# Kernel optimization log

Measured on AMD Instinct MI355X. Metric: run time of the kernel, lower is better.

## Reference

```python
import jax, jax.numpy as jnp
import numpy as np

TOP_K = 2
HEAD_NUM = 16


def setup_inputs() -> dict:
    key = jax.random.key(0)
    ks = jax.random.split(key, 6)
    B, H, N, D, G = 8, HEAD_NUM, 2048, 64, 128
    return {
        "q": jax.random.normal(ks[0], (B, H, N, D), dtype=jnp.float32),
        "k": jax.random.normal(ks[1], (B, H, N, D), dtype=jnp.float32),
        "v": jax.random.normal(ks[2], (B, H, N, D), dtype=jnp.float32),
        "gating_input": jax.random.normal(ks[3], (B, N, G), dtype=jnp.float32),
        "rank3_ninf_mask": jnp.zeros((B, N, N), dtype=jnp.float32),
        "W_gate": jax.random.normal(ks[4], (H, G), dtype=jnp.float32) * 0.02,
        "b_gate": jnp.zeros((H,), dtype=jnp.float32),
    }


def reference(q, k, v, gating_input, rank3_ninf_mask, W_gate, b_gate):
    B = q.shape[0]
    d = q.shape[-1]
    # --- router ---
    gate_logits = gating_input.mean(axis=1) @ W_gate.T + b_gate      # [B, H]
    gate_softmax = jax.nn.softmax(gate_logits, axis=1)               # [B, H]
    _, top_k_idx = jax.lax.top_k(gate_softmax, TOP_K)                # [B, K]
    gating_mask = jnp.zeros_like(gate_softmax).at[
        jnp.arange(B)[:, None], top_k_idx].set(1.0)
    # load balancing loss
    tokens_per_expert = gating_mask.sum(axis=0)                      # [H]
    density = tokens_per_expert / (tokens_per_expert.sum() + 1e-6)
    lb_loss = HEAD_NUM * jnp.sum(gate_softmax.mean(axis=0) * density)
    # --- gather selected heads: [B, K, N, D] ---
    idx = top_k_idx[:, :, None, None]
    q_sel = jnp.take_along_axis(q, idx, axis=1)
    k_sel = jnp.take_along_axis(k, idx, axis=1)
    v_sel = jnp.take_along_axis(v, idx, axis=1)
    # --- scaled dot attention ---
    score = jnp.einsum('bhqd,bhkd->bhqk', q_sel, k_sel) / jnp.sqrt(
        jnp.asarray(d, dtype=q.dtype))                               # [B,K,N,N]
    score = score + rank3_ninf_mask[:, None, :, :]
    weights = jax.nn.softmax(score, axis=3)
    out = jnp.einsum('bhqk,bhkd->bhqd', weights, v_sel)              # [B,K,N,D]
    B_, K_, N_, D_ = out.shape
    out = out.transpose(0, 2, 1, 3).reshape(B_, N_, K_ * D_)         # [B,N,K*D]
    return out, lb_loss
```

## Files before the change

### kernel.cpp

```cpp
#include <hip/hip_runtime.h>

#define NSEQ 2048
#define DH 64
#define NH 16
#define BKV 64
#define PSTRIDE 8448

typedef __attribute__((ext_vector_type(8))) short bf16x8;
typedef __attribute__((ext_vector_type(4))) short s16x4;
typedef __attribute__((ext_vector_type(4))) float f32x4;
typedef __attribute__((ext_vector_type(16))) float f32x16;
typedef __attribute__((ext_vector_type(4))) unsigned u32x4;

static __device__ __forceinline__ short f2bf(float f) {
    __bf16 b = (__bf16)f;
    return __builtin_bit_cast(short, b);
}

__global__ void gate_partial(const float* __restrict__ gi, float* __restrict__ wsA, int SL) {
    int b = blockIdx.x / SL, sl = blockIdx.x % SL;
    int rows = NSEQ / SL;
    int tid = threadIdx.x;
    int g = tid & 127, half = tid >> 7;
    float s = 0.f;
    int n0 = sl * rows;
    for (int n = n0 + half; n < n0 + rows; n += 2)
        s += gi[((size_t)b * NSEQ + n) * 128 + g];
    __shared__ float part[2][128];
    part[half][g] = s;
    __syncthreads();
    if (tid < 128) wsA[(b * SL + sl) * 128 + tid] = part[0][tid] + part[1][tid];
}

__global__ void gate_final(const float* __restrict__ wsA, const float* __restrict__ Wg,
                           const float* __restrict__ bg, float* __restrict__ ws_sm,
                           int* __restrict__ ws_idx, int SL) {
    int b = blockIdx.x, tid = threadIdx.x;
    __shared__ float meanv[128];
    __shared__ float logits[NH];
    if (tid < 128) {
        float s = 0.f;
        for (int sl = 0; sl < SL; ++sl) s += wsA[(b * SL + sl) * 128 + tid];
        meanv[tid] = s * (1.0f / NSEQ);
    }
    __syncthreads();
    if (tid < 128) {
        int h = tid >> 3, j = tid & 7;
        float p = 0.f;
        for (int i = 0; i < 16; ++i) { int g = j + 8 * i; p += meanv[g] * Wg[h * 128 + g]; }
        p += __shfl_xor(p, 1);
        p += __shfl_xor(p, 2);
        p += __shfl_xor(p, 4);
        if (j == 0) logits[h] = p + bg[h];
    }
    __syncthreads();
    if (tid == 0) {
        float mx = logits[0];
        for (int h = 1; h < NH; ++h) mx = fmaxf(mx, logits[h]);
        float e[NH], sum = 0.f;
        for (int h = 0; h < NH; ++h) { e[h] = __expf(logits[h] - mx); sum += e[h]; }
        float inv = 1.0f / sum;
        for (int h = 0; h < NH; ++h) ws_sm[b * NH + h] = e[h] * inv;
        int i1 = 0;
        for (int h = 1; h < NH; ++h) if (logits[h] > logits[i1]) i1 = h;
        int i2 = (i1 == 0) ? 1 : 0;
        for (int h = 0; h < NH; ++h) if (h != i1 && logits[h] > logits[i2]) i2 = h;
        ws_idx[b * 2 + 0] = i1;
        ws_idx[b * 2 + 1] = i2;
    }
}

static __device__ __forceinline__ void lb_compute(const float* ws_sm, const int* ws_idx,
                                                  float* out_lb) {
    float counts[NH];
    for (int h = 0; h < NH; ++h) counts[h] = 0.f;
    for (int i = 0; i < 16; ++i) counts[ws_idx[i]] += 1.0f;
    float lb = 0.f;
    for (int h = 0; h < NH; ++h) {
        float msm = 0.f;
        for (int b = 0; b < 8; ++b) msm += ws_sm[b * NH + h];
        msm *= (1.0f / 8.0f);
        lb += msm * (counts[h] / (16.0f + 1e-6f));
    }
    out_lb[0] = lb * (float)NH;
}

__global__ void lb_kernel(const float* __restrict__ ws_sm, const int* __restrict__ ws_idx,
                          float* __restrict__ out_lb) {
    if (threadIdx.x == 0 && blockIdx.x == 0) lb_compute(ws_sm, ws_idx, out_lb);
}

template<int SPLIT>
__global__ __launch_bounds__(256, 3)
void attn_kernel(const float* __restrict__ q, const float* __restrict__ k,
                 const float* __restrict__ v, const float* __restrict__ mask,
                 const int* __restrict__ topk, float* __restrict__ out,
                 float* __restrict__ part) {
    const int qt = blockIdx.x & 15;
    const int sp = blockIdx.x >> 4;
    const int kk = blockIdx.y;
    const int b  = blockIdx.z;
    const int hh = topk[b * 2 + kk];
    const int tid = threadIdx.x;
    const int wave = tid >> 6;
    const int lane = tid & 63;
    const int lq = lane & 31;
    const int hi = lane >> 5;

    const int nt = 32 / SPLIT;
    const int t_begin = sp * nt;

    __shared__ short Kb[64][72];
    __shared__ short Vt[64][72];
    __shared__ float scb[4][32];

    const float QSC = 0.125f * 1.4426950408889634f;
    const float MSC = 1.4426950408889634f;
    const float THR = 10.0f;

    const size_t headoff = ((size_t)b * NH + hh) * (size_t)NSEQ * DH;
    const int qbase = qt * 128 + wave * 32;

    bf16x8 qf[4];
    {
        const float* qp = q + headoff + (size_t)(qbase + lq) * DH;
        #pragma unroll
        for (int dk = 0; dk < 4; ++dk) {
            const float* p = qp + dk * 16 + hi * 8;
            float4 a = *(const float4*)p;
            float4 c = *(const float4*)(p + 4);
            bf16x8 f = { f2bf(a.x * QSC), f2bf(a.y * QSC), f2bf(a.z * QSC), f2bf(a.w * QSC),
                         f2bf(c.x * QSC), f2bf(c.y * QSC), f2bf(c.z * QSC), f2bf(c.w * QSC) };
            qf[dk] = f;
        }
    }

    f32x16 acc0, acc1;
    #pragma unroll
    for (int r = 0; r < 16; ++r) { acc0[r] = 0.f; acc1[r] = 0.f; }
    float m_r = -1e30f, l_r = 0.f;

    const float* kb = k + headoff;
    const float* vb = v + headoff;
    const float* mb = mask + (size_t)b * NSEQ * NSEQ + (size_t)(qbase + lq) * NSEQ;

    const int krow = tid >> 3;
    const int kcol = (tid & 7) * 8;
    const int vrow = (tid & 15) * 4;
    const int vcol = (tid >> 4) * 4;

    float4 kreg[4], vreg[4], mreg[8];

    auto issue_kv = [&](int t0) {
        const float* kp = kb + (size_t)(t0 + krow) * DH + kcol;
        kreg[0] = *(const float4*)kp;
        kreg[1] = *(const float4*)(kp + 4);
        kreg[2] = *(const float4*)(kp + 32 * DH);
        kreg[3] = *(const float4*)(kp + 32 * DH + 4);
        const float* vp = vb + (size_t)(t0 + vrow) * DH + vcol;
        #pragma unroll
        for (int i = 0; i < 4; ++i) vreg[i] = *(const float4*)(vp + i * DH);
    };
    auto issue_mask = [&](int t0) {
        const float* mp = mb + t0 + hi * 4;
        #pragma unroll
        for (int g = 0; g < 4; ++g) {
            mreg[g]     = *(const float4*)(mp + g * 8);
            mreg[4 + g] = *(const float4*)(mp + 32 + g * 8);
        }
    };

    auto pack2 = [&](float a, float bb) -> unsigned {
        union { short s[2]; unsigned u; } t;
        t.s[0] = f2bf(a); t.s[1] = f2bf(bb);
        return t.u;
    };
    auto buildfrag = [&](float a0, float a1, float a2, float a3,
                         float a4, float a5, float a6, float a7) -> bf16x8 {
        unsigned pk01 = pack2(a0, a1), pk23 = pack2(a2, a3);
        unsigned pk45 = pack2(a4, a5), pk67 = pack2(a6, a7);
        unsigned ta = hi ? pk01 : pk45;
        unsigned tb = hi ? pk23 : pk67;
        unsigned ya = __shfl_xor(ta, 32);
        unsigned yb = __shfl_xor(tb, 32);
        u32x4 fr = { hi ? ya : pk01, hi ? yb : pk23,
                     hi ? pk45 : ya, hi ? pk67 : yb };
        return __builtin_bit_cast(bf16x8, fr);
    };

    issue_kv(t_begin * BKV);
    issue_mask(t_begin * BKV);

    for (int t = 0; t < nt; ++t) {
        const int t0 = (t_begin + t) * BKV;
        __syncthreads();
        {
            bf16x8 k0 = { f2bf(kreg[0].x), f2bf(kreg[0].y), f2bf(kreg[0].z), f2bf(kreg[0].w),
                          f2bf(kreg[1].x), f2bf(kreg[1].y), f2bf(kreg[1].z), f2bf(kreg[1].w) };
            bf16x8 k1 = { f2bf(kreg[2].x), f2bf(kreg[2].y), f2bf(kreg[2].z), f2bf(kreg[2].w),
                          f2bf(kreg[3].x), f2bf(kreg[3].y), f2bf(kreg[3].z), f2bf(kreg[3].w) };
            *(bf16x8*)&Kb[krow][kcol] = k0;
            *(bf16x8*)&Kb[krow + 32][kcol] = k1;
            s16x4 c0v = { f2bf(vreg[0].x), f2bf(vreg[1].x), f2bf(vreg[2].x), f2bf(vreg[3].x) };
            s16x4 c1v = { f2bf(vreg[0].y), f2bf(vreg[1].y), f2bf(vreg[2].y), f2bf(vreg[3].y) };
            s16x4 c2v = { f2bf(vreg[0].z), f2bf(vreg[1].z), f2bf(vreg[2].z), f2bf(vreg[3].z) };
            s16x4 c3v = { f2bf(vreg[0].w), f2bf(vreg[1].w), f2bf(vreg[2].w), f2bf(vreg[3].w) };
            *(s16x4*)&Vt[vcol + 0][vrow] = c0v;
            *(s16x4*)&Vt[vcol + 1][vrow] = c1v;
            *(s16x4*)&Vt[vcol + 2][vrow] = c2v;
            *(s16x4*)&Vt[vcol + 3][vrow] = c3v;
        }
        __syncthreads();

        f32x16 S0, S1;
        #pragma unroll
        for (int r = 0; r < 16; ++r) { S0[r] = 0.f; S1[r] = 0.f; }
        #pragma unroll
        for (int dk = 0; dk < 4; ++dk) {
            bf16x8 kf0 = *(const bf16x8*)&Kb[lq][dk * 16 + hi * 8];
            bf16x8 kf1 = *(const bf16x8*)&Kb[32 + lq][dk * 16 + hi * 8];
            S0 = __builtin_amdgcn_mfma_f32_32x32x16_bf16(kf0, qf[dk], S0, 0, 0, 0);
            S1 = __builtin_amdgcn_mfma_f32_32x32x16_bf16(kf1, qf[dk], S1, 0, 0, 0);
        }
        #pragma unroll
        for (int g = 0; g < 4; ++g) {
            S0[4*g+0] = fmaf(mreg[g].x, MSC, S0[4*g+0]);
            S0[4*g+1] = fmaf(mreg[g].y, MSC, S0[4*g+1]);
            S0[4*g+2] = fmaf(mreg[g].z, MSC, S0[4*g+2]);
            S0[4*g+3] = fmaf(mreg[g].w, MSC, S0[4*g+3]);
            S1[4*g+0] = fmaf(mreg[4+g].x, MSC, S1[4*g+0]);
            S1[4*g+1] = fmaf(mreg[4+g].y, MSC, S1[4*g+1]);
            S1[4*g+2] = fmaf(mreg[4+g].z, MSC, S1[4*g+2]);
            S1[4*g+3] = fmaf(mreg[4+g].w, MSC, S1[4*g+3]);
        }

        if (t + 1 < nt) issue_kv(t0 + BKV);

        float tmx[16];
        #pragma unroll
        for (int r = 0; r < 16; ++r) tmx[r] = fmaxf(S0[r], S1[r]);
        #pragma unroll
        for (int w2 = 8; w2 > 0; w2 >>= 1)
            #pragma unroll
            for (int r = 0; r < 8; ++r) if (r < w2) tmx[r] = fmaxf(tmx[r], tmx[r + w2]);
        float pm = fmaxf(tmx[0], __shfl_xor(tmx[0], 32));

        if (__any(pm > m_r + THR)) {
            float mnew = fmaxf(m_r, pm);
            float scw = __builtin_amdgcn_exp2f(m_r - mnew);
            if (lane < 32) scb[wave][lane] = scw;
            #pragma unroll
            for (int g = 0; g < 4; ++g) {
                float4 s4 = *(const float4*)&scb[wave][hi * 4 + g * 8];
                acc0[4*g+0] *= s4.x; acc1[4*g+0] *= s4.x;
                acc0[4*g+1] *= s4.y; acc1[4*g+1] *= s4.y;
                acc0[4*g+2] *= s4.z; acc1[4*g+2] *= s4.z;
                acc0[4*g+3] *= s4.w; acc1[4*g+3] *= s4.w;
            }
            l_r *= scw; m_r = mnew;
        }
        float ps = 0.f;
        #pragma unroll
        for (int r = 0; r < 16; ++r) { float p = __builtin_amdgcn_exp2f(S0[r] - m_r); ps += p; S0[r] = p; }
        #pragma unroll
        for (int r = 0; r < 16; ++r) { float p = __builtin_amdgcn_exp2f(S1[r] - m_r); ps += p; S1[r] = p; }
        ps += __shfl_xor(ps, 32);
        l_r += ps;

        bf16x8 pf0 = buildfrag(S0[0], S0[1], S0[2],  S0[3],  S0[4],  S0[5],  S0[6],  S0[7]);
        bf16x8 pf1 = buildfrag(S0[8], S0[9], S0[10], S0[11], S0[12], S0[13], S0[14], S0[15]);
        bf16x8 pf2 = buildfrag(S1[0], S1[1], S1[2],  S1[3],  S1[4],  S1[5],  S1[6],  S1[7]);
        bf16x8 pf3 = buildfrag(S1[8], S1[9], S1[10], S1[11], S1[12], S1[13], S1[14], S1[15]);

        if (t + 1 < nt) issue_mask(t0 + BKV);

        #pragma unroll
        for (int c = 0; c < 4; ++c) {
            bf16x8 pf = (c == 0) ? pf0 : (c == 1) ? pf1 : (c == 2) ? pf2 : pf3;
            bf16x8 vf0 = *(const bf16x8*)&Vt[lq][c * 16 + hi * 8];
            bf16x8 vf1 = *(const bf16x8*)&Vt[32 + lq][c * 16 + hi * 8];
            acc0 = __builtin_amdgcn_mfma_f32_32x32x16_bf16(pf, vf0, acc0, 0, 0, 0);
            acc1 = __builtin_amdgcn_mfma_f32_32x32x16_bf16(pf, vf1, acc1, 0, 0, 0);
        }
    }

    if (SPLIT == 1) {
        if (lane < 32) scb[wave][lane] = 1.0f / l_r;
        #pragma unroll
        for (int g = 0; g < 4; ++g) {
            float4 s4 = *(const float4*)&scb[wave][hi * 4 + g * 8];
            #pragma unroll
            for (int j = 0; j < 4; ++j) {
                int qrow = qbase + hi * 4 + g * 8 + j;
                float sc = (j == 0) ? s4.x : (j == 1) ? s4.y : (j == 2) ? s4.z : s4.w;
                float* op = out + ((size_t)b * NSEQ + qrow) * 128 + kk * 64;
                op[lq]      = acc0[4*g+j] * sc;
                op[32 + lq] = acc1[4*g+j] * sc;
            }
        }
    } else {
        float* pp = part + (size_t)((((b * 2 + kk) * 16 + qt) * SPLIT) + sp) * PSTRIDE;
        #pragma unroll
        for (int g = 0; g < 4; ++g) {
            #pragma unroll
            for (int j = 0; j < 4; ++j) {
                int qloc = wave * 32 + hi * 4 + g * 8 + j;
                pp[qloc * 64 + lq]      = acc0[4*g+j];
                pp[qloc * 64 + 32 + lq] = acc1[4*g+j];
            }
        }
        if (lane < 32) {
            int wl = wave * 32 + lane;
            pp[8192 + wl] = m_r;
            pp[8320 + wl] = l_r;
        }
    }
}

__global__ __launch_bounds__(256)
void combine_kernel(const float* __restrict__ part, float* __restrict__ out,
                    const float* __restrict__ ws_sm, const int* __restrict__ ws_idx,
                    float* __restrict__ out_lb) {
    const int qt = blockIdx.x, kk = blockIdx.y, b = blockIdx.z;
    const float* base = part + (size_t)(((b * 2 + kk) * 16 + qt) * 4) * PSTRIDE;
    const int row = threadIdx.x >> 1;
    const int half = threadIdx.x & 1;

    float M = -1e30f;
    #pragma unroll
    for (int s = 0; s < 4; ++s) M = fmaxf(M, base[(size_t)s * PSTRIDE + 8192 + row]);

    float L = 0.f;
    float4 o[8];
    #pragma unroll
    for (int j = 0; j < 8; ++j) o[j] = make_float4(0.f, 0.f, 0.f, 0.f);

    #pragma unroll
    for (int s = 0; s < 4; ++s) {
        const float* pb = base + (size_t)s * PSTRIDE;
        float w = __builtin_amdgcn_exp2f(pb[8192 + row] - M);
        L += w * pb[8320 + row];
        const float4* ap = (const float4*)(pb + row * 64 + half * 32);
        #pragma unroll
        for (int j = 0; j < 8; ++j) {
            float4 a = ap[j];
            o[j].x += w * a.x; o[j].y += w * a.y;
            o[j].z += w * a.z; o[j].w += w * a.w;
        }
    }
    float inv = 1.0f / L;
    float* op = out + ((size_t)b * NSEQ + qt * 128 + row) * 128 + kk * 64 + half * 32;
    #pragma unroll
    for (int j = 0; j < 8; ++j) {
        float4 r = make_float4(o[j].x * inv, o[j].y * inv, o[j].z * inv, o[j].w * inv);
        ((float4*)op)[j] = r;
    }
    if (qt == 0 && kk == 0 && b == 0 && threadIdx.x == 0)
        lb_compute(ws_sm, ws_idx, out_lb);
}

extern "C" void kernel_launch(void* const* d_in, const int* in_sizes, int n_in,
                              void* d_out, int out_size, void* d_ws, size_t ws_size,
                              hipStream_t stream) {
    const float* q    = (const float*)d_in[0];
    const float* k    = (const float*)d_in[1];
    const float* v    = (const float*)d_in[2];
    const float* gi   = (const float*)d_in[3];
    const float* mask = (const float*)d_in[4];
    const float* Wg   = (const float*)d_in[5];
    const float* bg   = (const float*)d_in[6];
    float* out = (float*)d_out;
    float* out_lb = out + (size_t)8 * NSEQ * 128;

    const size_t part_bytes = (size_t)1024 * PSTRIDE * 4;
    const size_t gateA_bytes = (size_t)8 * 64 * 128 * 4 + 4096;
    const size_t needA = part_bytes + gateA_bytes;
    const size_t needB = 65536 + part_bytes;

    int SL, SPLIT;
    float* ws_part;
    float* wsA;
    if (ws_size >= needA) {
        SL = 64; SPLIT = 4;
        ws_part = (float*)d_ws;
        wsA = (float*)((char*)d_ws + part_bytes);
    } else if (ws_size >= needB) {
        SL = 8; SPLIT = 4;
        wsA = (float*)d_ws;
        ws_part = (float*)((char*)d_ws + 65536);
    } else {
        SL = 8; SPLIT = 1;
        wsA = (float*)d_ws;
        ws_part = (float*)d_ws;
    }
    float* ws_sm = wsA + 8 * SL * 128;
    int*   ws_idx = (int*)(ws_sm + 8 * NH);

    gate_partial<<<8 * SL, 256, 0, stream>>>(gi, wsA, SL);
    gate_final<<<8, 256, 0, stream>>>(wsA, Wg, bg, ws_sm, ws_idx, SL);

    if (SPLIT == 4) {
        dim3 grid(16 * 4, 2, 8);
        attn_kernel<4><<<grid, 256, 0, stream>>>(q, k, v, mask, ws_idx, out, ws_part);
        dim3 cgrid(16, 2, 8);
        combine_kernel<<<cgrid, 256, 0, stream>>>(ws_part, out, ws_sm, ws_idx, out_lb);
    } else {
        lb_kernel<<<1, 64, 0, stream>>>(ws_sm, ws_idx, out_lb);
        dim3 grid(16, 2, 8);
        attn_kernel<1><<<grid, 256, 0, stream>>>(q, k, v, mask, ws_idx, out, ws_part);
    }
}
```

Baseline: 117.7 us.

## Add split-8 KV partitioning, raise occupancy bound, and hoist mask prefetch

```diff
diff --git a/kernel.cpp b/kernel.cpp
--- a/kernel.cpp
+++ b/kernel.cpp
@@ -91,7 +91,7 @@
 }
 
 template<int SPLIT>
-__global__ __launch_bounds__(256, 3)
+__global__ __launch_bounds__(256, 4)
 void attn_kernel(const float* __restrict__ q, const float* __restrict__ k,
                  const float* __restrict__ v, const float* __restrict__ mask,
                  const int* __restrict__ topk, float* __restrict__ out,
@@ -234,7 +234,7 @@
             S1[4*g+3] = fmaf(mreg[4+g].w, MSC, S1[4*g+3]);
         }
 
-        if (t + 1 < nt) issue_kv(t0 + BKV);
+        if (t + 1 < nt) { issue_kv(t0 + BKV); issue_mask(t0 + BKV); }
 
         float tmx[16];
         #pragma unroll
@@ -272,8 +272,6 @@
         bf16x8 pf2 = buildfrag(S1[0], S1[1], S1[2],  S1[3],  S1[4],  S1[5],  S1[6],  S1[7]);
         bf16x8 pf3 = buildfrag(S1[8], S1[9], S1[10], S1[11], S1[12], S1[13], S1[14], S1[15]);
 
-        if (t + 1 < nt) issue_mask(t0 + BKV);
-
         #pragma unroll
         for (int c = 0; c < 4; ++c) {
             bf16x8 pf = (c == 0) ? pf0 : (c == 1) ? pf1 : (c == 2) ? pf2 : pf3;
@@ -317,18 +315,19 @@
     }
 }
 
+template<int SPLIT>
 __global__ __launch_bounds__(256)
 void combine_kernel(const float* __restrict__ part, float* __restrict__ out,
                     const float* __restrict__ ws_sm, const int* __restrict__ ws_idx,
                     float* __restrict__ out_lb) {
     const int qt = blockIdx.x, kk = blockIdx.y, b = blockIdx.z;
-    const float* base = part + (size_t)(((b * 2 + kk) * 16 + qt) * 4) * PSTRIDE;
+    const float* base = part + (size_t)(((b * 2 + kk) * 16 + qt) * SPLIT) * PSTRIDE;
     const int row = threadIdx.x >> 1;
     const int half = threadIdx.x & 1;
 
     float M = -1e30f;
     #pragma unroll
-    for (int s = 0; s < 4; ++s) M = fmaxf(M, base[(size_t)s * PSTRIDE + 8192 + row]);
+    for (int s = 0; s < SPLIT; ++s) M = fmaxf(M, base[(size_t)s * PSTRIDE + 8192 + row]);
 
     float L = 0.f;
     float4 o[8];
@@ -336,7 +335,7 @@
     for (int j = 0; j < 8; ++j) o[j] = make_float4(0.f, 0.f, 0.f, 0.f);
 
     #pragma unroll
-    for (int s = 0; s < 4; ++s) {
+    for (int s = 0; s < SPLIT; ++s) {
         const float* pb = base + (size_t)s * PSTRIDE;
         float w = __builtin_amdgcn_exp2f(pb[8192 + row] - M);
         L += w * pb[8320 + row];
@@ -372,18 +371,24 @@
     float* out = (float*)d_out;
     float* out_lb = out + (size_t)8 * NSEQ * 128;
 
-    const size_t part_bytes = (size_t)1024 * PSTRIDE * 4;
     const size_t gateA_bytes = (size_t)8 * 64 * 128 * 4 + 4096;
-    const size_t needA = part_bytes + gateA_bytes;
-    const size_t needB = 65536 + part_bytes;
+    const size_t part8 = (size_t)2048 * PSTRIDE * 4;
+    const size_t part4 = (size_t)1024 * PSTRIDE * 4;
+    const size_t need8 = part8 + gateA_bytes;
+    const size_t need4 = part4 + gateA_bytes;
+    const size_t needB = 65536 + part4;
 
     int SL, SPLIT;
     float* ws_part;
     float* wsA;
-    if (ws_size >= needA) {
+    if (ws_size >= need8) {
+        SL = 64; SPLIT = 8;
+        ws_part = (float*)d_ws;
+        wsA = (float*)((char*)d_ws + part8);
+    } else if (ws_size >= need4) {
         SL = 64; SPLIT = 4;
         ws_part = (float*)d_ws;
-        wsA = (float*)((char*)d_ws + part_bytes);
+        wsA = (float*)((char*)d_ws + part4);
     } else if (ws_size >= needB) {
         SL = 8; SPLIT = 4;
         wsA = (float*)d_ws;
@@ -399,11 +404,15 @@
     gate_partial<<<8 * SL, 256, 0, stream>>>(gi, wsA, SL);
     gate_final<<<8, 256, 0, stream>>>(wsA, Wg, bg, ws_sm, ws_idx, SL);
 
-    if (SPLIT == 4) {
+    dim3 cgrid(16, 2, 8);
+    if (SPLIT == 8) {
+        dim3 grid(16 * 8, 2, 8);
+        attn_kernel<8><<<grid, 256, 0, stream>>>(q, k, v, mask, ws_idx, out, ws_part);
+        combine_kernel<8><<<cgrid, 256, 0, stream>>>(ws_part, out, ws_sm, ws_idx, out_lb);
+    } else if (SPLIT == 4) {
         dim3 grid(16 * 4, 2, 8);
         attn_kernel<4><<<grid, 256, 0, stream>>>(q, k, v, mask, ws_idx, out, ws_part);
-        dim3 cgrid(16, 2, 8);
-        combine_kernel<<<cgrid, 256, 0, stream>>>(ws_part, out, ws_sm, ws_idx, out_lb);
+        combine_kernel<4><<<cgrid, 256, 0, stream>>>(ws_part, out, ws_sm, ws_idx, out_lb);
     } else {
         lb_kernel<<<1, 64, 0, stream>>>(ws_sm, ws_idx, out_lb);
         dim3 grid(16, 2, 8);
```

Measured after the change: 218.4 us. 1.86x slower.

## Double query tile to 256 rows with 512-thread blocks sharing K/V tiles

Applied to the files above, without the earlier changes.

```diff
diff --git a/kernel.cpp b/kernel.cpp
--- a/kernel.cpp
+++ b/kernel.cpp
@@ -4,11 +4,11 @@
 #define DH 64
 #define NH 16
 #define BKV 64
-#define PSTRIDE 8448
+#define BQ 256
+#define PSTRIDE 16896
 
 typedef __attribute__((ext_vector_type(8))) short bf16x8;
 typedef __attribute__((ext_vector_type(4))) short s16x4;
-typedef __attribute__((ext_vector_type(4))) float f32x4;
 typedef __attribute__((ext_vector_type(16))) float f32x16;
 typedef __attribute__((ext_vector_type(4))) unsigned u32x4;
 
@@ -91,13 +91,13 @@
 }
 
 template<int SPLIT>
-__global__ __launch_bounds__(256, 3)
+__global__ __launch_bounds__(512, 4)
 void attn_kernel(const float* __restrict__ q, const float* __restrict__ k,
                  const float* __restrict__ v, const float* __restrict__ mask,
                  const int* __restrict__ topk, float* __restrict__ out,
                  float* __restrict__ part) {
-    const int qt = blockIdx.x & 15;
-    const int sp = blockIdx.x >> 4;
+    const int qt = blockIdx.x & 7;
+    const int sp = blockIdx.x >> 3;
     const int kk = blockIdx.y;
     const int b  = blockIdx.z;
     const int hh = topk[b * 2 + kk];
@@ -112,14 +112,14 @@
 
     __shared__ short Kb[64][72];
     __shared__ short Vt[64][72];
-    __shared__ float scb[4][32];
+    __shared__ float scb[8][32];
 
     const float QSC = 0.125f * 1.4426950408889634f;
     const float MSC = 1.4426950408889634f;
     const float THR = 10.0f;
 
     const size_t headoff = ((size_t)b * NH + hh) * (size_t)NSEQ * DH;
-    const int qbase = qt * 128 + wave * 32;
+    const int qbase = qt * BQ + wave * 32;
 
     bf16x8 qf[4];
     {
@@ -147,19 +147,19 @@
     const int krow = tid >> 3;
     const int kcol = (tid & 7) * 8;
     const int vrow = (tid & 15) * 4;
-    const int vcol = (tid >> 4) * 4;
-
-    float4 kreg[4], vreg[4], mreg[8];
+    const int vcol = (tid >> 4) * 2;
+
+    float4 kreg[2];
+    float2 vreg[4];
+    float4 mreg[8];
 
     auto issue_kv = [&](int t0) {
         const float* kp = kb + (size_t)(t0 + krow) * DH + kcol;
         kreg[0] = *(const float4*)kp;
         kreg[1] = *(const float4*)(kp + 4);
-        kreg[2] = *(const float4*)(kp + 32 * DH);
-        kreg[3] = *(const float4*)(kp + 32 * DH + 4);
         const float* vp = vb + (size_t)(t0 + vrow) * DH + vcol;
         #pragma unroll
-        for (int i = 0; i < 4; ++i) vreg[i] = *(const float4*)(vp + i * DH);
+        for (int i = 0; i < 4; ++i) vreg[i] = *(const float2*)(vp + i * DH);
     };
     auto issue_mask = [&](int t0) {
         const float* mp = mb + t0 + hi * 4;
@@ -197,18 +197,11 @@
         {
             bf16x8 k0 = { f2bf(kreg[0].x), f2bf(kreg[0].y), f2bf(kreg[0].z), f2bf(kreg[0].w),
                           f2bf(kreg[1].x), f2bf(kreg[1].y), f2bf(kreg[1].z), f2bf(kreg[1].w) };
-            bf16x8 k1 = { f2bf(kreg[2].x), f2bf(kreg[2].y), f2bf(kreg[2].z), f2bf(kreg[2].w),
-                          f2bf(kreg[3].x), f2bf(kreg[3].y), f2bf(kreg[3].z), f2bf(kreg[3].w) };
             *(bf16x8*)&Kb[krow][kcol] = k0;
-            *(bf16x8*)&Kb[krow + 32][kcol] = k1;
             s16x4 c0v = { f2bf(vreg[0].x), f2bf(vreg[1].x), f2bf(vreg[2].x), f2bf(vreg[3].x) };
             s16x4 c1v = { f2bf(vreg[0].y), f2bf(vreg[1].y), f2bf(vreg[2].y), f2bf(vreg[3].y) };
-            s16x4 c2v = { f2bf(vreg[0].z), f2bf(vreg[1].z), f2bf(vreg[2].z), f2bf(vreg[3].z) };
-            s16x4 c3v = { f2bf(vreg[0].w), f2bf(vreg[1].w), f2bf(vreg[2].w), f2bf(vreg[3].w) };
             *(s16x4*)&Vt[vcol + 0][vrow] = c0v;
             *(s16x4*)&Vt[vcol + 1][vrow] = c1v;
-            *(s16x4*)&Vt[vcol + 2][vrow] = c2v;
-            *(s16x4*)&Vt[vcol + 3][vrow] = c3v;
         }
         __syncthreads();
 
@@ -299,7 +292,7 @@
             }
         }
     } else {
-        float* pp = part + (size_t)((((b * 2 + kk) * 16 + qt) * SPLIT) + sp) * PSTRIDE;
+        float* pp = part + (size_t)((((b * 2 + kk) * 8 + qt) * SPLIT) + sp) * PSTRIDE;
         #pragma unroll
         for (int g = 0; g < 4; ++g) {
             #pragma unroll
@@ -311,24 +304,28 @@
         }
         if (lane < 32) {
             int wl = wave * 32 + lane;
-            pp[8192 + wl] = m_r;
-            pp[8320 + wl] = l_r;
-        }
-    }
-}
-
+            pp[16384 + wl] = m_r;
+            pp[16640 + wl] = l_r;
+        }
+    }
+}
+
+template<int SPLIT>
 __global__ __launch_bounds__(256)
 void combine_kernel(const float* __restrict__ part, float* __restrict__ out,
                     const float* __restrict__ ws_sm, const int* __restrict__ ws_idx,
                     float* __restrict__ out_lb) {
-    const int qt = blockIdx.x, kk = blockIdx.y, b = blockIdx.z;
-    const float* base = part + (size_t)(((b * 2 + kk) * 16 + qt) * 4) * PSTRIDE;
-    const int row = threadIdx.x >> 1;
+    const int qt128 = blockIdx.x;
+    const int kk = blockIdx.y, b = blockIdx.z;
+    const int pq = qt128 >> 1;
+    const int rbase = (qt128 & 1) * 128;
+    const float* base = part + (size_t)(((b * 2 + kk) * 8 + pq) * SPLIT) * PSTRIDE;
+    const int row = rbase + (threadIdx.x >> 1);
     const int half = threadIdx.x & 1;
 
     float M = -1e30f;
     #pragma unroll
-    for (int s = 0; s < 4; ++s) M = fmaxf(M, base[(size_t)s * PSTRIDE + 8192 + row]);
+    for (int s = 0; s < SPLIT; ++s) M = fmaxf(M, base[(size_t)s * PSTRIDE + 16384 + row]);
 
     float L = 0.f;
     float4 o[8];
@@ -336,10 +333,10 @@
     for (int j = 0; j < 8; ++j) o[j] = make_float4(0.f, 0.f, 0.f, 0.f);
 
     #pragma unroll
-    for (int s = 0; s < 4; ++s) {
+    for (int s = 0; s < SPLIT; ++s) {
         const float* pb = base + (size_t)s * PSTRIDE;
-        float w = __builtin_amdgcn_exp2f(pb[8192 + row] - M);
-        L += w * pb[8320 + row];
+        float w = __builtin_amdgcn_exp2f(pb[16384 + row] - M);
+        L += w * pb[16640 + row];
         const float4* ap = (const float4*)(pb + row * 64 + half * 32);
         #pragma unroll
         for (int j = 0; j < 8; ++j) {
@@ -349,13 +346,13 @@
         }
     }
     float inv = 1.0f / L;
-    float* op = out + ((size_t)b * NSEQ + qt * 128 + row) * 128 + kk * 64 + half * 32;
+    float* op = out + ((size_t)b * NSEQ + pq * BQ + row) * 128 + kk * 64 + half * 32;
     #pragma unroll
     for (int j = 0; j < 8; ++j) {
         float4 r = make_float4(o[j].x * inv, o[j].y * inv, o[j].z * inv, o[j].w * inv);
         ((float4*)op)[j] = r;
     }
-    if (qt == 0 && kk == 0 && b == 0 && threadIdx.x == 0)
+    if (qt128 == 0 && kk == 0 && b == 0 && threadIdx.x == 0)
         lb_compute(ws_sm, ws_idx, out_lb);
 }
 
@@ -372,18 +369,18 @@
     float* out = (float*)d_out;
     float* out_lb = out + (size_t)8 * NSEQ * 128;
 
-    const size_t part_bytes = (size_t)1024 * PSTRIDE * 4;
     const size_t gateA_bytes = (size_t)8 * 64 * 128 * 4 + 4096;
-    const size_t needA = part_bytes + gateA_bytes;
-    const size_t needB = 65536 + part_bytes;
+    const size_t part4 = (size_t)512 * PSTRIDE * 4;
+    const size_t need4 = part4 + gateA_bytes;
+    const size_t needB = 65536 + part4;
 
     int SL, SPLIT;
     float* ws_part;
     float* wsA;
-    if (ws_size >= needA) {
+    if (ws_size >= need4) {
         SL = 64; SPLIT = 4;
         ws_part = (float*)d_ws;
-        wsA = (float*)((char*)d_ws + part_bytes);
+        wsA = (float*)((char*)d_ws + part4);
     } else if (ws_size >= needB) {
         SL = 8; SPLIT = 4;
         wsA = (float*)d_ws;
@@ -400,13 +397,13 @@
     gate_final<<<8, 256, 0, stream>>>(wsA, Wg, bg, ws_sm, ws_idx, SL);
 
     if (SPLIT == 4) {
-        dim3 grid(16 * 4, 2, 8);
-        attn_kernel<4><<<grid, 256, 0, stream>>>(q, k, v, mask, ws_idx, out, ws_part);
+        dim3 grid(8 * 4, 2, 8);
+        attn_kernel<4><<<grid, 512, 0, stream>>>(q, k, v, mask, ws_idx, out, ws_part);
         dim3 cgrid(16, 2, 8);
-        combine_kernel<<<cgrid, 256, 0, stream>>>(ws_part, out, ws_sm, ws_idx, out_lb);
+        combine_kernel<4><<<cgrid, 256, 0, stream>>>(ws_part, out, ws_sm, ws_idx, out_lb);
     } else {
         lb_kernel<<<1, 64, 0, stream>>>(ws_sm, ws_idx, out_lb);
-        dim3 grid(16, 2, 8);
-        attn_kernel<1><<<grid, 256, 0, stream>>>(q, k, v, mask, ws_idx, out, ws_part);
-    }
-}
+        dim3 grid(8, 2, 8);
+        attn_kernel<1><<<grid, 512, 0, stream>>>(q, k, v, mask, ws_idx, out, ws_part);
+    }
+}
```

Result: slower. 139.0 us (+18.0%).
